# Kernel tuning notes

Measured on AMD Instinct MI355X. Metric: run time of the kernel, lower is better.

## Reference

```python
import jax, jax.numpy as jnp
import numpy as np

N = 2048      # n_nodes
D = 512       # n_channels
AVG_DEG = 16  # average graph degree


def setup_inputs() -> dict:
    key = jax.random.key(0)
    k1, k2, k3 = jax.random.split(key, 3)
    # node features [N, D]
    x = jax.random.normal(k1, (N, D), dtype=jnp.float32)
    # random symmetric graph -> combinatorial Laplacian L = D - A
    E = N * AVG_DEG
    src = jax.random.randint(k2, (E,), 0, N)
    dst = jax.random.randint(k3, (E,), 0, N)
    A = jnp.zeros((N, N), jnp.float32).at[src, dst].add(1.0)
    A = (A + A.T) * 0.5
    A = A * (1.0 - jnp.eye(N, dtype=jnp.float32))  # drop self loops
    deg = A.sum(axis=1)
    L = jnp.diag(deg) - A
    # learned diffusion time (scalar parameter, ic=0.5)
    t = jnp.float32(0.5)
    return {"x": x, "L": L, "t": t}


def reference(x, L, t):
    # forward clamps diffusion_time to >= 1e-8
    tt = jnp.maximum(t, jnp.float32(1e-8))
    # heat kernel: expm(-t * L); the original loops over channels applying
    # compute_diffusion(x[:, [i]], t, L, 'matrix_exp') == expm(-t L) @ x[:, i],
    # which is exactly one dense matmul fused across all channels.
    P = jax.scipy.linalg.expm(-tt * L)  # [N, N]
    return P @ x  # [N, D]
```

## Files before the change

### kernel.cpp

```cpp
#include <hip/hip_runtime.h>

#define N_NODES 2048
#define N_CH    512
#define K_CHEB  48
#define NNZ_MAX 131072
#define NB      256

#define OFF_DIAG   0
#define OFF_SCAL   8192
#define OFF_PERM   12288
#define OFF_BASE   20480
#define OFF_CNTO   28672
#define OFF_GCNT   36864
#define OFF_BND    36868
#define OFF_PKV    40960

#define PAD_OFF    16384u

__device__ __forceinline__ float b2f(unsigned short u) {
    return __uint_as_float(((unsigned int)u) << 16);
}
__device__ __forceinline__ bool detect32(const unsigned int* tw) {
    return (tw[0] & 0xFFFFu) == 0u;
}

__global__ void __launch_bounds__(256)
k_prep(const void* __restrict__ Lp, const unsigned int* __restrict__ tw,
       float* __restrict__ diagv, int* __restrict__ basev, int* __restrict__ cnto,
       int* __restrict__ gcnt, unsigned short* __restrict__ pkv) {
    __shared__ unsigned short stage[4][N_NODES];
    __shared__ int scnt[4];
    __shared__ int sbase;
    int w    = threadIdx.x >> 6;
    int lane = threadIdx.x & 63;
    int row  = blockIdx.x * 4 + w;
    bool is32 = detect32(tw);
    int run = 0; float dv = 0.f;
    if (is32) {
        const float4* rf4 = (const float4*)((const float*)Lp + (size_t)row * N_NODES);
        #pragma unroll
        for (int i = 0; i < 8; i++) {
            int j = i * 64 + lane;
            float4 v = rf4[j];
            if (j == (row >> 2)) {
                int rm = row & 3;
                if      (rm == 0) { dv = v.x; v.x = 0.f; }
                else if (rm == 1) { dv = v.y; v.y = 0.f; }
                else if (rm == 2) { dv = v.z; v.z = 0.f; }
                else              { dv = v.w; v.w = 0.f; }
            }
            int c0 = j * 4;
            int n0 = (v.x != 0.f) ? (int)(-2.0f * v.x + 0.5f) : 0;
            int n1 = (v.y != 0.f) ? (int)(-2.0f * v.y + 0.5f) : 0;
            int n2 = (v.z != 0.f) ? (int)(-2.0f * v.z + 0.5f) : 0;
            int n3 = (v.w != 0.f) ? (int)(-2.0f * v.w + 0.5f) : 0;
            int tn = n0 + n1 + n2 + n3;
            int xs = tn;
            #pragma unroll
            for (int d = 1; d < 64; d <<= 1) { int q = __shfl_up(xs, d); if (lane >= d) xs += q; }
            int o = run + xs - tn;
            for (int q = 0; q < n0; q++) stage[w][o++] = (unsigned short)((c0 + 0) << 3);
            for (int q = 0; q < n1; q++) stage[w][o++] = (unsigned short)((c0 + 1) << 3);
            for (int q = 0; q < n2; q++) stage[w][o++] = (unsigned short)((c0 + 2) << 3);
            for (int q = 0; q < n3; q++) stage[w][o++] = (unsigned short)((c0 + 3) << 3);
            run += __shfl(xs, 63);
        }
    } else {
        const unsigned short* rp = (const unsigned short*)Lp + (size_t)row * N_NODES;
        for (int c0 = 0; c0 < N_NODES; c0 += 64) {
            float v = b2f(rp[c0 + lane]);
            int n = 0;
            if (c0 + lane == row) dv = v;
            else if (v != 0.f)    n = (int)(-2.0f * v + 0.5f);
            int xs = n;
            #pragma unroll
            for (int d = 1; d < 64; d <<= 1) { int q = __shfl_up(xs, d); if (lane >= d) xs += q; }
            int o = run + xs - n;
            for (int q = 0; q < n; q++) stage[w][o + q] = (unsigned short)((c0 + lane) << 3);
            run += __shfl(xs, 63);
        }
    }
    #pragma unroll
    for (int o = 32; o; o >>= 1) dv += __shfl_xor(dv, o);
    int padded = (run + 7) & ~7;
    for (int e = run + lane; e < padded; e += 64) stage[w][e] = (unsigned short)PAD_OFF;
    if (lane == 0) scnt[w] = padded;
    __syncthreads();
    if (threadIdx.x == 0)
        sbase = atomicAdd(gcnt, scnt[0] + scnt[1] + scnt[2] + scnt[3]);
    __syncthreads();
    int myb = sbase;
    for (int w2 = 0; w2 < w; w2++) myb += scnt[w2];
    if (lane == 0) { basev[row] = myb; cnto[row] = padded >> 3; diagv[row] = dv; }
    const unsigned int* s32 = (const unsigned int*)stage[w];
    unsigned int* p32 = (unsigned int*)pkv + (myb >> 1);
    for (int i = lane; i < (padded >> 1); i += 64) p32[i] = s32[i];
}

__global__ void __launch_bounds__(256)
k_bound(const float* __restrict__ diagv, const int* __restrict__ basev,
        const int* __restrict__ cnto, const unsigned short* __restrict__ pkv,
        unsigned int* __restrict__ bnd) {
    __shared__ float wmax[4];
    int w    = threadIdx.x >> 6;
    int lane = threadIdx.x & 63;
    int r    = blockIdx.x * 4 + w;
    float d = diagv[r];
    float mb = 0.f;
    if (d > 0.f) {
        const unsigned short* pe = pkv + basev[r];
        int cnt = cnto[r] << 3;
        float s = 0.f;
        for (int e = lane; e < cnt; e += 64) {
            unsigned int u = pe[e];
            if (u < PAD_OFF) s += diagv[u >> 3];
        }
        #pragma unroll
        for (int o = 32; o; o >>= 1) s += __shfl_xor(s, o);
        mb = d + 0.5f * s / d;
    }
    if (lane == 0) wmax[w] = mb;
    __syncthreads();
    if (threadIdx.x == 0) {
        float m = fmaxf(fmaxf(wmax[0], wmax[1]), fmaxf(wmax[2], wmax[3]));
        atomicMax(bnd, __float_as_uint(m));
    }
}

__global__ void k_scan(const float* __restrict__ diagv, float* __restrict__ scal,
                       const void* __restrict__ tp, const int* __restrict__ cnto,
                       const unsigned int* __restrict__ bnd,
                       int* __restrict__ perm) {
    __shared__ float  fmaxs[256];
    __shared__ double dz[1];
    __shared__ float  cabs[K_CHEB + 1];
    __shared__ int    hist[256];
    __shared__ int    hstart[256];
    int t = threadIdx.x;
    hist[t] = 0;
    float mx = 0.f;
    #pragma unroll
    for (int i = 0; i < 8; i++) mx = fmaxf(mx, diagv[t * 8 + i]);
    fmaxs[t] = mx;
    __syncthreads();
    for (int o = 128; o; o >>= 1) {
        if (t < o) fmaxs[t] = fmaxf(fmaxs[t], fmaxs[t + o]);
        __syncthreads();
    }
    if (t == 0) {
        bool is32 = detect32((const unsigned int*)tp);
        float tt = is32 ? ((const float*)tp)[0] : b2f(((const unsigned short*)tp)[0]);
        tt = fmaxf(tt, 1e-8f);
        float beta = 2.0f * fmaxs[0];
        float bM   = __uint_as_float(bnd[0]) * 1.00002f + 1e-7f;
        if (bM > 0.f && bM < beta) beta = bM;
        scal[0] = (beta > 0.f) ? 2.0f / beta : 0.f;
        dz[0] = (beta > 0.f) ? (double)tt * (double)beta * 0.5 : 0.0;
    }
    __syncthreads();
    if (t <= K_CHEB) {
        int k = t;
        double z = dz[0];
        double emz = exp(-z), h = 0.5 * z, h2 = h * h;
        double term = 1.0;
        for (int j = 1; j <= k; j++) term *= h / (double)j;
        double sum = term;
        for (int m = 1; m < 300; m++) {
            term *= h2 / ((double)m * (double)(m + k));
            sum += term;
            if (term == 0.0 || term < sum * 1e-18) break;
        }
        double ck = emz * sum * (k == 0 ? 1.0 : 2.0);
        if (k & 1) ck = -ck;
        scal[16 + k] = (float)ck;
        cabs[k] = (float)fabs(ck);
    }
    __syncthreads();
    if (t == 0) {
        int keff = 1;
        for (int k = K_CHEB; k >= 2; k--)
            if (cabs[k] >= 2.5e-4f) { keff = k; break; }
        scal[1] = (float)keff;
    }
    #pragma unroll
    for (int i = 0; i < 8; i++) {
        int q = min(cnto[t * 8 + i], 255);
        atomicAdd(&hist[q], 1);
    }
    __syncthreads();
    if (t == 0) {
        int acc = 0;
        for (int l = 255; l >= 0; l--) { hstart[l] = acc; acc += hist[l]; }
    }
    __syncthreads();
    #pragma unroll
    for (int i = 0; i < 8; i++) {
        int idx = t * 8 + i;
        int q = min(cnto[idx], 255);
        int pos = atomicAdd(&hstart[q], 1);
        perm[pos] = idx;
    }
}

__global__ void __launch_bounds__(256)
k_sort(const int* __restrict__ basev, const int* __restrict__ cnto,
       const int* __restrict__ perm, unsigned short* __restrict__ pkv) {
    int w    = threadIdx.x >> 6;
    int lane = threadIdx.x & 63;
    int q    = blockIdx.x * 4 + w;
    int t    = (q < 1024) ? q : (2047 - q);
    unsigned int phi = (unsigned int)(t & 15);
    int r    = perm[q];
    int cnt  = cnto[r] << 3;
    unsigned short* pe = pkv + basev[r];
    unsigned long long below = (1ull << lane) - 1ull;
    for (int c0 = 0; c0 < cnt; c0 += 64) {
        int n = cnt - c0; if (n > 64) n = 64;
        bool act = lane < n;
        unsigned int u = act ? (unsigned int)pe[c0 + lane] : 0u;
        int kb = (int)(((u >> 3) - phi) & 15u);
        int rank = 0;
        #pragma unroll
        for (int kk = 0; kk < 16; kk++) {
            unsigned long long m = __ballot(act && (kb == kk));
            if (kk == kb) rank = __popcll(m & below);
        }
        int dest = 0;
        #pragma unroll
        for (int kk = 0; kk < 16; kk++) {
            unsigned long long m = __ballot(act && (kb == kk));
            int c = __popcll(m);
            dest += (c < rank) ? c : rank;
            if (kk < kb && c > rank) dest++;
        }
        if (act) pe[c0 + dest] = (unsigned short)u;
    }
}

__device__ __forceinline__ void oct_acc(const float2* __restrict__ cur, uint4 q,
                                        float& ax, float& ay, float& bx, float& by) {
    const char* cb = (const char*)cur;
    #pragma unroll
    for (int i = 0; i < 4; i++) {
        unsigned int u = (i == 0) ? q.x : (i == 1) ? q.y : (i == 2) ? q.z : q.w;
        float2 c0 = *(const float2*)(cb + (u & 0xFFFFu));
        float2 c1 = *(const float2*)(cb + (u >> 16));
        ax += c0.x; ay += c0.y;
        bx += c1.x; by += c1.y;
    }
}

__device__ __forceinline__ float2 gatherR(const float2* __restrict__ cur,
                                          const uint4* __restrict__ s4,
                                          int j0, int j1) {
    float ax = 0.f, ay = 0.f, bx = 0.f, by = 0.f;
    int j = j0;
    if (j + 2 <= j1) {
        uint4 q0 = s4[j], q1 = s4[j + 1];
        j += 2;
        while (j + 2 <= j1) {
            uint4 p0 = s4[j], p1 = s4[j + 1];
            oct_acc(cur, q0, ax, ay, bx, by);
            oct_acc(cur, q1, ax, ay, bx, by);
            q0 = p0; q1 = p1;
            j += 2;
        }
        oct_acc(cur, q0, ax, ay, bx, by);
        oct_acc(cur, q1, ax, ay, bx, by);
    }
    if (j < j1) oct_acc(cur, s4[j], ax, ay, bx, by);
    return make_float2(ax + bx, ay + by);
}

__global__ void __launch_bounds__(1024, 4)
k_cheb(const void* __restrict__ x, const unsigned int* __restrict__ tw,
       const int* __restrict__ basev, const int* __restrict__ cnto,
       const float* __restrict__ diagv, const unsigned short* __restrict__ pkv,
       const float* __restrict__ scal, const int* __restrict__ perm,
       void* __restrict__ out) {
    __shared__ float2 bufA[N_NODES + 8];
    __shared__ float2 bufB[N_NODES + 8];
    __shared__ float  scoef[K_CHEB + 1];
    int t  = threadIdx.x;
    int cb = blockIdx.x * 2;
    bool is32 = detect32(tw);
    if (t <= K_CHEB) scoef[t] = scal[16 + t];
    if (t == 0) {
        bufA[N_NODES] = make_float2(0.f, 0.f);
        bufB[N_NODES] = make_float2(0.f, 0.f);
    }
    int ra = perm[t], rb = perm[2047 - t];
    int na = cnto[ra], nb = cnto[rb];
    int ja = basev[ra] >> 3, jb = basev[rb] >> 3;
    const uint4* s4 = (const uint4*)pkv;
    float da = diagv[ra], db = diagv[rb];
    float g = scal[0];
    int   K = (int)scal[1];

    float2 xa, xb;
    if (is32) {
        xa = *(const float2*)((const float*)x + (size_t)ra * N_CH + cb);
        xb = *(const float2*)((const float*)x + (size_t)rb * N_CH + cb);
    } else {
        const unsigned short* xp = (const unsigned short*)x;
        unsigned int wa = *(const unsigned int*)(xp + (size_t)ra * N_CH + cb);
        unsigned int wb = *(const unsigned int*)(xp + (size_t)rb * N_CH + cb);
        xa = make_float2(b2f((unsigned short)(wa & 0xFFFFu)), b2f((unsigned short)(wa >> 16)));
        xb = make_float2(b2f((unsigned short)(wb & 0xFFFFu)), b2f((unsigned short)(wb >> 16)));
    }
    bufA[ra] = xa; bufA[rb] = xb;
    __syncthreads();

    float gm = -0.5f * g;
    float ia = g * da - 1.f, ib = g * db - 1.f;
    float2 aa = gatherR(bufA, s4, ja, ja + na);
    float2 ab = gatherR(bufA, s4, jb, jb + nb);
    float2 pva = xa, pvb = xb;
    float2 cua = make_float2(gm * aa.x + ia * xa.x, gm * aa.y + ia * xa.y);
    float2 cub = make_float2(gm * ab.x + ib * xb.x, gm * ab.y + ib * xb.y);
    float c0 = scoef[0], c1 = scoef[1];
    float2 oa = make_float2(c0 * xa.x + c1 * cua.x, c0 * xa.y + c1 * cua.y);
    float2 ob = make_float2(c0 * xb.x + c1 * cub.x, c0 * xb.y + c1 * cub.y);
    bufB[ra] = cua; bufB[rb] = cub;
    __syncthreads();

    float gn  = -g;
    float dga = 2.f * g * da - 2.f, dgb = 2.f * g * db - 2.f;

#define CHEB_STEP(RD, WR)                                                  \
    {   float ck = scoef[k];                                               \
        float2 ba = gatherR(RD, s4, ja, ja + na);                          \
        float2 bb = gatherR(RD, s4, jb, jb + nb);                          \
        float2 tna = make_float2(gn * ba.x + dga * cua.x - pva.x,          \
                                 gn * ba.y + dga * cua.y - pva.y);         \
        float2 tnb = make_float2(gn * bb.x + dgb * cub.x - pvb.x,          \
                                 gn * bb.y + dgb * cub.y - pvb.y);         \
        pva = cua; cua = tna;                                              \
        pvb = cub; cub = tnb;                                              \
        oa.x += ck * tna.x; oa.y += ck * tna.y;                            \
        ob.x += ck * tnb.x; ob.y += ck * tnb.y;                            \
        WR[ra] = tna; WR[rb] = tnb;                                        \
        __syncthreads(); }

    int k = 2;
    while (k <= K) {
        CHEB_STEP(bufB, bufA)
        k++;
        if (k > K) break;
        CHEB_STEP(bufA, bufB)
        k++;
    }
#undef CHEB_STEP

    if (is32) {
        *(float2*)((float*)out + (size_t)ra * N_CH + cb) = oa;
        *(float2*)((float*)out + (size_t)rb * N_CH + cb) = ob;
    } else {
        unsigned int ua, ub;
        { unsigned int u0 = __float_as_uint(oa.x), u1 = __float_as_uint(oa.y);
          u0 = (u0 + 0x7FFFu + ((u0 >> 16) & 1u)) >> 16;
          u1 = (u1 + 0x7FFFu + ((u1 >> 16) & 1u)) >> 16;
          ua = u0 | (u1 << 16); }
        { unsigned int u0 = __float_as_uint(ob.x), u1 = __float_as_uint(ob.y);
          u0 = (u0 + 0x7FFFu + ((u0 >> 16) & 1u)) >> 16;
          u1 = (u1 + 0x7FFFu + ((u1 >> 16) & 1u)) >> 16;
          ub = u0 | (u1 << 16); }
        *(unsigned int*)((unsigned short*)out + (size_t)ra * N_CH + cb) = ua;
        *(unsigned int*)((unsigned short*)out + (size_t)rb * N_CH + cb) = ub;
    }
}

extern "C" void kernel_launch(void* const* d_in, const int* in_sizes, int n_in,
                              void* d_out, int out_size, void* d_ws, size_t ws_size,
                              hipStream_t stream) {
    const void* x  = d_in[0];
    const void* L  = d_in[1];
    const void* tp = d_in[2];
    const unsigned int* tw = (const unsigned int*)tp;

    char* ws = (char*)d_ws;
    float*          diagv = (float*)          (ws + OFF_DIAG);
    float*          scal  = (float*)          (ws + OFF_SCAL);
    int*            perm  = (int*)            (ws + OFF_PERM);
    int*            basev = (int*)            (ws + OFF_BASE);
    int*            cnto  = (int*)            (ws + OFF_CNTO);
    int*            gcnt  = (int*)            (ws + OFF_GCNT);
    unsigned int*   bnd   = (unsigned int*)   (ws + OFF_BND);
    unsigned short* pkv   = (unsigned short*) (ws + OFF_PKV);

    hipMemsetAsync(gcnt, 0, 8, stream);
    k_prep<<<512, 256, 0, stream>>>(L, tw, diagv, basev, cnto, gcnt, pkv);
    k_bound<<<512, 256, 0, stream>>>(diagv, basev, cnto, pkv, bnd);
    k_scan<<<1,   256, 0, stream>>>(diagv, scal, tp, cnto, bnd, perm);
    k_sort<<<512, 256, 0, stream>>>(basev, cnto, perm, pkv);
    k_cheb<<<NB, 1024, 0, stream>>>(x, tw, basev, cnto, diagv, pkv, scal, perm, d_out);
}
```

Measured before the change: 183.6 us.

## Split shared-memory Chebyshev buffers into per-channel planes to cut LDS bank conflicts

Moves the LDS vectors from interleaved float2 per node to a blocked layout where each 128-node group stores its x channel and y channel 128 floats apart. The packed neighbour offsets are re-encoded to match, the diagonal lookup in the bound kernel is decoded accordingly, and the per-row neighbour sort now spreads entries over 32 banks instead of 16. The goal is fewer bank conflicts in the gather-heavy recurrence. In exchange each gather issues two 32-bit loads instead of one 64-bit load, and the sort kernel does twice as many ballot rounds.

```diff
diff --git a/kernel.cpp b/kernel.cpp
--- a/kernel.cpp
+++ b/kernel.cpp
@@ -15,7 +15,9 @@
 #define OFF_BND    36868
 #define OFF_PKV    40960
 
+#define ENC_ROW(c) ((unsigned short)((((c) >> 7) << 10) | (((c) & 127) << 2)))
 #define PAD_OFF    16384u
+#define BUF_DW     4352
 
 __device__ __forceinline__ float b2f(unsigned short u) {
     return __uint_as_float(((unsigned int)u) << 16);
@@ -59,10 +61,10 @@
             #pragma unroll
             for (int d = 1; d < 64; d <<= 1) { int q = __shfl_up(xs, d); if (lane >= d) xs += q; }
             int o = run + xs - tn;
-            for (int q = 0; q < n0; q++) stage[w][o++] = (unsigned short)((c0 + 0) << 3);
-            for (int q = 0; q < n1; q++) stage[w][o++] = (unsigned short)((c0 + 1) << 3);
-            for (int q = 0; q < n2; q++) stage[w][o++] = (unsigned short)((c0 + 2) << 3);
-            for (int q = 0; q < n3; q++) stage[w][o++] = (unsigned short)((c0 + 3) << 3);
+            for (int q = 0; q < n0; q++) stage[w][o++] = ENC_ROW(c0 + 0);
+            for (int q = 0; q < n1; q++) stage[w][o++] = ENC_ROW(c0 + 1);
+            for (int q = 0; q < n2; q++) stage[w][o++] = ENC_ROW(c0 + 2);
+            for (int q = 0; q < n3; q++) stage[w][o++] = ENC_ROW(c0 + 3);
             run += __shfl(xs, 63);
         }
     } else {
@@ -76,7 +78,7 @@
             #pragma unroll
             for (int d = 1; d < 64; d <<= 1) { int q = __shfl_up(xs, d); if (lane >= d) xs += q; }
             int o = run + xs - n;
-            for (int q = 0; q < n; q++) stage[w][o + q] = (unsigned short)((c0 + lane) << 3);
+            for (int q = 0; q < n; q++) stage[w][o + q] = ENC_ROW(c0 + lane);
             run += __shfl(xs, 63);
         }
     }
@@ -113,7 +115,10 @@
         float s = 0.f;
         for (int e = lane; e < cnt; e += 64) {
             unsigned int u = pe[e];
-            if (u < PAD_OFF) s += diagv[u >> 3];
+            if (u < PAD_OFF) {
+                unsigned int dw = u >> 2;
+                s += diagv[((dw >> 8) << 7) | (dw & 127u)];
+            }
         }
         #pragma unroll
         for (int o = 32; o; o >>= 1) s += __shfl_xor(s, o);
@@ -209,7 +214,7 @@
     int lane = threadIdx.x & 63;
     int q    = blockIdx.x * 4 + w;
     int t    = (q < 1024) ? q : (2047 - q);
-    unsigned int phi = (unsigned int)(t & 15);
+    unsigned int phi = (unsigned int)(t & 31);
     int r    = perm[q];
     int cnt  = cnto[r] << 3;
     unsigned short* pe = pkv + basev[r];
@@ -218,16 +223,16 @@
         int n = cnt - c0; if (n > 64) n = 64;
         bool act = lane < n;
         unsigned int u = act ? (unsigned int)pe[c0 + lane] : 0u;
-        int kb = (int)(((u >> 3) - phi) & 15u);
+        int kb = (int)((((u >> 2) & 31u) - phi) & 31u);
         int rank = 0;
         #pragma unroll
-        for (int kk = 0; kk < 16; kk++) {
+        for (int kk = 0; kk < 32; kk++) {
             unsigned long long m = __ballot(act && (kb == kk));
             if (kk == kb) rank = __popcll(m & below);
         }
         int dest = 0;
         #pragma unroll
-        for (int kk = 0; kk < 16; kk++) {
+        for (int kk = 0; kk < 32; kk++) {
             unsigned long long m = __ballot(act && (kb == kk));
             int c = __popcll(m);
             dest += (c < rank) ? c : rank;
@@ -237,20 +242,23 @@
     }
 }
 
-__device__ __forceinline__ void oct_acc(const float2* __restrict__ cur, uint4 q,
+__device__ __forceinline__ void oct_acc(const float* __restrict__ cur, uint4 q,
                                         float& ax, float& ay, float& bx, float& by) {
     const char* cb = (const char*)cur;
     #pragma unroll
     for (int i = 0; i < 4; i++) {
         unsigned int u = (i == 0) ? q.x : (i == 1) ? q.y : (i == 2) ? q.z : q.w;
-        float2 c0 = *(const float2*)(cb + (u & 0xFFFFu));
-        float2 c1 = *(const float2*)(cb + (u >> 16));
-        ax += c0.x; ay += c0.y;
-        bx += c1.x; by += c1.y;
-    }
-}
-
-__device__ __forceinline__ float2 gatherR(const float2* __restrict__ cur,
+        unsigned int o0 = u & 0xFFFFu, o1 = u >> 16;
+        float c0x = *(const float*)(cb + o0);
+        float c0y = *(const float*)(cb + o0 + 512);
+        float c1x = *(const float*)(cb + o1);
+        float c1y = *(const float*)(cb + o1 + 512);
+        ax += c0x; ay += c0y;
+        bx += c1x; by += c1y;
+    }
+}
+
+__device__ __forceinline__ float2 gatherR(const float* __restrict__ cur,
                                           const uint4* __restrict__ s4,
                                           int j0, int j1) {
     float ax = 0.f, ay = 0.f, bx = 0.f, by = 0.f;
@@ -278,20 +286,22 @@
        const float* __restrict__ diagv, const unsigned short* __restrict__ pkv,
        const float* __restrict__ scal, const int* __restrict__ perm,
        void* __restrict__ out) {
-    __shared__ float2 bufA[N_NODES + 8];
-    __shared__ float2 bufB[N_NODES + 8];
-    __shared__ float  scoef[K_CHEB + 1];
+    __shared__ float bufA[BUF_DW];
+    __shared__ float bufB[BUF_DW];
+    __shared__ float scoef[K_CHEB + 1];
     int t  = threadIdx.x;
     int cb = blockIdx.x * 2;
     bool is32 = detect32(tw);
     if (t <= K_CHEB) scoef[t] = scal[16 + t];
     if (t == 0) {
-        bufA[N_NODES] = make_float2(0.f, 0.f);
-        bufB[N_NODES] = make_float2(0.f, 0.f);
+        bufA[4096] = 0.f; bufA[4224] = 0.f;
+        bufB[4096] = 0.f; bufB[4224] = 0.f;
     }
     int ra = perm[t], rb = perm[2047 - t];
     int na = cnto[ra], nb = cnto[rb];
     int ja = basev[ra] >> 3, jb = basev[rb] >> 3;
+    int sa = ((ra >> 7) << 8) | (ra & 127);
+    int sb = ((rb >> 7) << 8) | (rb & 127);
     const uint4* s4 = (const uint4*)pkv;
     float da = diagv[ra], db = diagv[rb];
     float g = scal[0];
@@ -308,7 +318,8 @@
         xa = make_float2(b2f((unsigned short)(wa & 0xFFFFu)), b2f((unsigned short)(wa >> 16)));
         xb = make_float2(b2f((unsigned short)(wb & 0xFFFFu)), b2f((unsigned short)(wb >> 16)));
     }
-    bufA[ra] = xa; bufA[rb] = xb;
+    bufA[sa] = xa.x; bufA[sa + 128] = xa.y;
+    bufA[sb] = xb.x; bufA[sb + 128] = xb.y;
     __syncthreads();
 
     float gm = -0.5f * g;
@@ -321,7 +332,8 @@
     float c0 = scoef[0], c1 = scoef[1];
     float2 oa = make_float2(c0 * xa.x + c1 * cua.x, c0 * xa.y + c1 * cua.y);
     float2 ob = make_float2(c0 * xb.x + c1 * cub.x, c0 * xb.y + c1 * cub.y);
-    bufB[ra] = cua; bufB[rb] = cub;
+    bufB[sa] = cua.x; bufB[sa + 128] = cua.y;
+    bufB[sb] = cub.x; bufB[sb + 128] = cub.y;
     __syncthreads();
 
     float gn  = -g;
@@ -339,7 +351,8 @@
         pvb = cub; cub = tnb;                                              \
         oa.x += ck * tna.x; oa.y += ck * tna.y;                            \
         ob.x += ck * tnb.x; ob.y += ck * tnb.y;                            \
-        WR[ra] = tna; WR[rb] = tnb;                                        \
+        WR[sa] = tna.x; WR[sa + 128] = tna.y;                              \
+        WR[sb] = tnb.x; WR[sb + 128] = tnb.y;                              \
         __syncthreads(); }
 
     int k = 2;
```

Result: slower. 209.8 us (+14.2%).
